# Optimization experiments

Measured on AMD Instinct MI355X. Metric: run time of the kernel, lower is better.

Reference implementation:

```python
import jax, jax.numpy as jnp
import numpy as np

N = 50000
E = 800000
IN_DIM = 256
HID = 64
HEADS = 4
OUT_DIM = 32
NEG_SLOPE = 0.2
EPS = 1e-5


def segment_softmax(logits, seg, num_segments):
    # logits: [E, H]; softmax over edges sharing the same destination node
    m = jax.ops.segment_max(logits, seg, num_segments=num_segments)
    m = jnp.where(jnp.isfinite(m), m, 0.0)
    e = jnp.exp(logits - m[seg])
    s = jax.ops.segment_sum(e, seg, num_segments=num_segments)
    return e / (s[seg] + 1e-16)


def setup_inputs() -> dict:
    key = jax.random.key(0)
    ks = jax.random.split(key, 16)
    d = {}
    d['x'] = jax.random.normal(ks[0], (N, IN_DIM), dtype=jnp.float32)
    d['edge_index'] = jax.random.randint(ks[1], (2, E), 0, N, dtype=jnp.int64)
    sc = lambda fan: 1.0 / np.sqrt(fan)
    # input transform: Linear(256->128), Linear(128->64)
    d['t1_w'] = jax.random.normal(ks[2], (IN_DIM, IN_DIM // 2), dtype=jnp.float32) * sc(IN_DIM)
    d['t1_b'] = jnp.zeros((IN_DIM // 2,), jnp.float32)
    d['t2_w'] = jax.random.normal(ks[3], (IN_DIM // 2, IN_DIM // 4), dtype=jnp.float32) * sc(IN_DIM // 2)
    d['t2_b'] = jnp.zeros((IN_DIM // 4,), jnp.float32)
    d['g1_w'] = jax.random.normal(ks[4], (IN_DIM // 4, HEADS * HID), dtype=jnp.float32) * sc(IN_DIM // 4)
    d['g1_att_src'] = jax.random.normal(ks[5], (HEADS, HID), dtype=jnp.float32) * sc(HID)
    d['g1_att_dst'] = jax.random.normal(ks[6], (HEADS, HID), dtype=jnp.float32) * sc(HID)
    d['g1_b'] = jnp.zeros((HEADS * HID,), jnp.float32)
    # GraphNorm(256)
    d['gn_w'] = jnp.ones((HEADS * HID,), jnp.float32)
    d['gn_b'] = jnp.zeros((HEADS * HID,), jnp.float32)
    d['gn_ms'] = jnp.ones((HEADS * HID,), jnp.float32)
    # GATConv 2: 256 -> 32, 1 head, no concat (mean == identity for 1 head)
    d['g2_w'] = jax.random.normal(ks[7], (HEADS * HID, OUT_DIM), dtype=jnp.float32) * sc(HEADS * HID)
    d['g2_att_src'] = jax.random.normal(ks[8], (1, OUT_DIM), dtype=jnp.float32) * sc(OUT_DIM)
    d['g2_att_dst'] = jax.random.normal(ks[9], (1, OUT_DIM), dtype=jnp.float32) * sc(OUT_DIM)
    d['g2_b'] = jnp.zeros((OUT_DIM,), jnp.float32)
    return d


def gat_conv(x, src, dst, w, att_src, att_dst, bias, n_nodes):
    heads, ch = att_src.shape
    h = (x @ w).reshape(n_nodes, heads, ch)            # [N,H,C]
    a_src = jnp.sum(h * att_src, axis=-1)              # [N,H]
    a_dst = jnp.sum(h * att_dst, axis=-1)              # [N,H]
    logits = jax.nn.leaky_relu(a_src[src] + a_dst[dst], NEG_SLOPE)  # [E,H]
    alpha = segment_softmax(logits, dst, n_nodes)      # [E,H]
    msgs = alpha[:, :, None] * h[src]                  # [E,H,C]
    out = jax.ops.segment_sum(msgs, dst, num_segments=n_nodes)  # [N,H,C]
    return out.reshape(n_nodes, heads * ch) + bias


def reference(x, edge_index, t1_w, t1_b, t2_w, t2_b,
              g1_w, g1_att_src, g1_att_dst, g1_b,
              gn_w, gn_b, gn_ms,
              g2_w, g2_att_src, g2_att_dst, g2_b):
    src, dst = edge_index[0], edge_index[1]
    # input transform (dropout inactive in eval)
    h = jax.nn.relu(x @ t1_w + t1_b)
    h = jax.nn.relu(h @ t2_w + t2_b)
    # GAT layer 1 (concat heads)
    h = gat_conv(h, src, dst, g1_w, g1_att_src, g1_att_dst, g1_b, N)
    # GraphNorm over the whole graph (batch=None -> single graph)
    mean = jnp.mean(h, axis=0)
    o = h - mean * gn_ms
    var = jnp.mean(o * o, axis=0)
    h = o / jnp.sqrt(var + EPS) * gn_w + gn_b
    h = jax.nn.elu(h)
    # GAT layer 2 (1 head, concat=False)
    h = gat_conv(h, src, dst, g2_w, g2_att_src, g2_att_dst, g2_b, N)
    return jax.nn.log_softmax(h, axis=1)
```

## Files before the change

### kernel.cpp

```cpp
#include <hip/hip_runtime.h>

#define NSLOPE 0.2f
#define GEPS 1e-5f

typedef unsigned short ushortT;
typedef __attribute__((ext_vector_type(8))) unsigned short us8;
typedef __attribute__((ext_vector_type(8))) __bf16 bf16x8;
typedef __attribute__((ext_vector_type(4))) float f32x4;

__device__ __forceinline__ float lrelu(float x) { return x >= 0.f ? x : NSLOPE * x; }
__device__ __forceinline__ ushortT f2bf(float f) {
    unsigned int u = __float_as_uint(f);
    return (ushortT)((u + 0x7fffu + ((u >> 16) & 1u)) >> 16);
}
__device__ __forceinline__ float bf2f(ushortT h) {
    return __uint_as_float((unsigned int)h << 16);
}
__device__ __forceinline__ ushortT f2h(float f) {
    union { _Float16 h; ushortT u; } v; v.h = (_Float16)f; return v.u;
}
__device__ __forceinline__ float h2f(ushortT u) {
    union { _Float16 h; ushortT u; } v; v.u = u; return (float)v.h;
}

__global__ __launch_bounds__(256) void k_prep_hist(
    const float* __restrict__ w1, const float* __restrict__ w2,
    const float* __restrict__ g1w, const float* __restrict__ g2w,
    ushortT* __restrict__ w1t, ushortT* __restrict__ w2t,
    ushortT* __restrict__ g1t, ushortT* __restrict__ g2t,
    const int* __restrict__ dst, int* __restrict__ deg, int E)
{
    if (blockIdx.x >= 128) {
        const int i = (blockIdx.x - 128) * 256 + threadIdx.x;
        if (i < E) atomicAdd(&deg[dst[i]], 1);
        return;
    }
    const int i = blockIdx.x * 256 + threadIdx.x;
    if (i < 128 * 256) { const int c = i >> 8, k = i & 255; w1t[i] = f2bf(w1[k * 128 + c]); }
    if (i < 64 * 128)  { const int c = i >> 7, k = i & 127; w2t[i] = f2bf(w2[k * 64 + c]); }
    if (i < 256 * 64)  { const int c = i >> 6, k = i & 63;  g1t[i] = f2bf(g1w[k * 256 + c]); }
    if (i < 32 * 256)  { const int c = i >> 8, k = i & 255; g2t[i] = f2bf(g2w[k * 32 + c]); }
}

__global__ __launch_bounds__(256) void k_lin1(const float* __restrict__ x,
    const ushortT* __restrict__ w1t, const float* __restrict__ b1,
    ushortT* __restrict__ h1, int n,
    const int* __restrict__ deg, int* __restrict__ offs, int* __restrict__ bsum, int gemmB)
{
    if ((int)blockIdx.x >= gemmB) {
        __shared__ int sm[256];
        const int t = threadIdx.x;
        const int i = (blockIdx.x - gemmB) * 256 + t;
        const int v = (i < n) ? deg[i] : 0;
        sm[t] = v;
        __syncthreads();
        for (int off = 1; off < 256; off <<= 1) {
            int add = (t >= off) ? sm[t - off] : 0;
            __syncthreads();
            sm[t] += add;
            __syncthreads();
        }
        if (i < n) offs[i] = sm[t] - v;
        if (t == 255) bsum[blockIdx.x - gemmB] = sm[255];
        return;
    }
    __shared__ us8 Ab[64 * 128 / 16];
    __shared__ us8 Bb[128 * 128 / 16];
    char* A = (char*)Ab; char* B = (char*)Bb;
    const int t = threadIdx.x;
    const int w = t >> 6, l = t & 63;
    const int lo = l & 15, hi = l >> 4;
    const int n0 = blockIdx.x * 64;
    const int wm = (w >> 1) * 32, wn = (w & 1) * 64;
    f32x4 acc[2][4];
    #pragma unroll
    for (int mf = 0; mf < 2; ++mf)
        #pragma unroll
        for (int nf = 0; nf < 4; ++nf) acc[mf][nf] = (f32x4){0.f, 0.f, 0.f, 0.f};

    const int arow = t >> 2, ak0 = (t & 3) * 16;
    int agn = n0 + arow; if (agn >= n) agn = n - 1;
    const int asw = (arow & 7) << 4;

    for (int kc = 0; kc < 4; ++kc) {
        __syncthreads();
        {
            ushortT tmp[16];
            const float* xp = &x[(size_t)agn * 256 + kc * 64 + ak0];
            #pragma unroll
            for (int j = 0; j < 4; ++j) {
                const float4 v = *(const float4*)(xp + j * 4);
                tmp[j*4+0] = f2bf(v.x); tmp[j*4+1] = f2bf(v.y);
                tmp[j*4+2] = f2bf(v.z); tmp[j*4+3] = f2bf(v.w);
            }
            *(us8*)(A + arow * 128 + ((ak0 * 2) ^ asw)) = *(us8*)tmp;
            *(us8*)(A + arow * 128 + ((ak0 * 2 + 16) ^ asw)) = *(us8*)(tmp + 8);
        }
        #pragma unroll
        for (int i = 0; i < 4; ++i) {
            const int idx = i * 256 + t, br = idx >> 3, bs = idx & 7;
            const us8 v = *(const us8*)&w1t[(size_t)br * 256 + kc * 64 + bs * 8];
            *(us8*)(B + br * 128 + ((bs * 16) ^ ((br & 7) << 4))) = v;
        }
        __syncthreads();
        #pragma unroll
        for (int ks = 0; ks < 2; ++ks) {
            const int koff = ks * 64 + hi * 16;
            bf16x8 af[2], bf[4];
            #pragma unroll
            for (int mf = 0; mf < 2; ++mf) {
                const int r = wm + mf * 16 + lo;
                af[mf] = *(const bf16x8*)(A + r * 128 + (koff ^ ((r & 7) << 4)));
            }
            #pragma unroll
            for (int nf = 0; nf < 4; ++nf) {
                const int r = wn + nf * 16 + lo;
                bf[nf] = *(const bf16x8*)(B + r * 128 + (koff ^ ((r & 7) << 4)));
            }
            #pragma unroll
            for (int mf = 0; mf < 2; ++mf)
                #pragma unroll
                for (int nf = 0; nf < 4; ++nf)
                    acc[mf][nf] = __builtin_amdgcn_mfma_f32_16x16x32_bf16(af[mf], bf[nf], acc[mf][nf], 0, 0, 0);
        }
    }
    #pragma unroll
    for (int nf = 0; nf < 4; ++nf) {
        const int col = wn + nf * 16 + lo;
        const float bb = b1[col];
        #pragma unroll
        for (int mf = 0; mf < 2; ++mf)
            #pragma unroll
            for (int j = 0; j < 4; ++j) {
                const int r = n0 + wm + mf * 16 + hi * 4 + j;
                if (r < n) h1[(size_t)r * 128 + col] = f2bf(fmaxf(acc[mf][nf][j] + bb, 0.f));
            }
    }
}

__global__ __launch_bounds__(256) void k_lin2(const ushortT* __restrict__ h1,
    const ushortT* __restrict__ w2t, const float* __restrict__ b2,
    ushortT* __restrict__ h2, int n,
    int* __restrict__ bsum, int nb, int gemmB)
{
    if ((int)blockIdx.x >= gemmB) {
        __shared__ int sm[256];
        const int t = threadIdx.x;
        const int v = (t < nb) ? bsum[t] : 0;
        sm[t] = v;
        __syncthreads();
        for (int off = 1; off < 256; off <<= 1) {
            int add = (t >= off) ? sm[t - off] : 0;
            __syncthreads();
            sm[t] += add;
            __syncthreads();
        }
        if (t < nb) bsum[t] = sm[t] - v;
        return;
    }
    __shared__ us8 Ab[64 * 128 / 16];
    __shared__ us8 Bb[64 * 128 / 16];
    char* A = (char*)Ab; char* B = (char*)Bb;
    const int t = threadIdx.x;
    const int w = t >> 6, l = t & 63;
    const int lo = l & 15, hi = l >> 4;
    const int n0 = blockIdx.x * 64;
    const int wm = (w >> 1) * 32, wn = (w & 1) * 32;
    f32x4 acc[2][2];
    #pragma unroll
    for (int mf = 0; mf < 2; ++mf)
        #pragma unroll
        for (int nf = 0; nf < 2; ++nf) acc[mf][nf] = (f32x4){0.f, 0.f, 0.f, 0.f};

    const int arow = t >> 2, ak0 = (t & 3) * 16;
    int agn = n0 + arow; if (agn >= n) agn = n - 1;
    const int asw = (arow & 7) << 4;

    for (int kc = 0; kc < 2; ++kc) {
        __syncthreads();
        {
            const us8 v0 = *(const us8*)&h1[(size_t)agn * 128 + kc * 64 + ak0];
            const us8 v1 = *(const us8*)&h1[(size_t)agn * 128 + kc * 64 + ak0 + 8];
            *(us8*)(A + arow * 128 + ((ak0 * 2) ^ asw)) = v0;
            *(us8*)(A + arow * 128 + ((ak0 * 2 + 16) ^ asw)) = v1;
        }
        #pragma unroll
        for (int i = 0; i < 2; ++i) {
            const int idx = i * 256 + t, br = idx >> 3, bs = idx & 7;
            const us8 v = *(const us8*)&w2t[(size_t)br * 128 + kc * 64 + bs * 8];
            *(us8*)(B + br * 128 + ((bs * 16) ^ ((br & 7) << 4))) = v;
        }
        __syncthreads();
        #pragma unroll
        for (int ks = 0; ks < 2; ++ks) {
            const int koff = ks * 64 + hi * 16;
            bf16x8 af[2], bf[2];
            #pragma unroll
            for (int mf = 0; mf < 2; ++mf) {
                const int r = wm + mf * 16 + lo;
                af[mf] = *(const bf16x8*)(A + r * 128 + (koff ^ ((r & 7) << 4)));
            }
            #pragma unroll
            for (int nf = 0; nf < 2; ++nf) {
                const int r = wn + nf * 16 + lo;
                bf[nf] = *(const bf16x8*)(B + r * 128 + (koff ^ ((r & 7) << 4)));
            }
            #pragma unroll
            for (int mf = 0; mf < 2; ++mf)
                #pragma unroll
                for (int nf = 0; nf < 2; ++nf)
                    acc[mf][nf] = __builtin_amdgcn_mfma_f32_16x16x32_bf16(af[mf], bf[nf], acc[mf][nf], 0, 0, 0);
        }
    }
    #pragma unroll
    for (int nf = 0; nf < 2; ++nf) {
        const int col = wn + nf * 16 + lo;
        const float bb = b2[col];
        #pragma unroll
        for (int mf = 0; mf < 2; ++mf)
            #pragma unroll
            for (int j = 0; j < 4; ++j) {
                const int r = n0 + wm + mf * 16 + hi * 4 + j;
                if (r < n) h2[(size_t)r * 64 + col] = f2bf(fmaxf(acc[mf][nf][j] + bb, 0.f));
            }
    }
}

__global__ __launch_bounds__(256) void k_g1feat(const ushortT* __restrict__ h2,
    const ushortT* __restrict__ g1t, const float* __restrict__ attS, const float* __restrict__ attD,
    ushortT* __restrict__ hg1, float* __restrict__ a1s, float* __restrict__ a1d, int n,
    int* __restrict__ offs, int* __restrict__ cursor, const int* __restrict__ bsum, int E, int gemmB)
{
    if ((int)blockIdx.x >= gemmB) {
        const int sb = blockIdx.x - gemmB;
        const int i = sb * 256 + threadIdx.x;
        if (i < n) {
            int o = offs[i] + bsum[i >> 8];
            offs[i] = o;
            cursor[i] = o;
        }
        if (i == 0) offs[n] = E;
        return;
    }
    __shared__ us8 Ab[64 * 128 / 16];
    __shared__ us8 Bb[256 * 128 / 16];
    char* A = (char*)Ab; char* B = (char*)Bb;
    const int t = threadIdx.x;
    const int w = t >> 6, l = t & 63;
    const int lo = l & 15, hi = l >> 4;
    const int n0 = blockIdx.x * 64;
    const int wm = (w >> 1) * 32, wn = (w & 1) * 128;
    f32x4 acc[2][8];
    #pragma unroll
    for (int mf = 0; mf < 2; ++mf)
        #pragma unroll
        for (int nf = 0; nf < 8; ++nf) acc[mf][nf] = (f32x4){0.f, 0.f, 0.f, 0.f};

    {
        const int arow = t >> 2, ak0 = (t & 3) * 16;
        int agn = n0 + arow; if (agn >= n) agn = n - 1;
        const int asw = (arow & 7) << 4;
        const us8 v0 = *(const us8*)&h2[(size_t)agn * 64 + ak0];
        const us8 v1 = *(const us8*)&h2[(size_t)agn * 64 + ak0 + 8];
        *(us8*)(A + arow * 128 + ((ak0 * 2) ^ asw)) = v0;
        *(us8*)(A + arow * 128 + ((ak0 * 2 + 16) ^ asw)) = v1;
    }
    #pragma unroll
    for (int i = 0; i < 8; ++i) {
        const int idx = i * 256 + t, br = idx >> 3, bs = idx & 7;
        const us8 v = *(const us8*)&g1t[(size_t)br * 64 + bs * 8];
        *(us8*)(B + br * 128 + ((bs * 16) ^ ((br & 7) << 4))) = v;
    }
    __syncthreads();
    #pragma unroll
    for (int ks = 0; ks < 2; ++ks) {
        const int koff = ks * 64 + hi * 16;
        bf16x8 af[2];
        #pragma unroll
        for (int mf = 0; mf < 2; ++mf) {
            const int r = wm + mf * 16 + lo;
            af[mf] = *(const bf16x8*)(A + r * 128 + (koff ^ ((r & 7) << 4)));
        }
        #pragma unroll
        for (int nf = 0; nf < 8; ++nf) {
            const int r = wn + nf * 16 + lo;
            const bf16x8 bf = *(const bf16x8*)(B + r * 128 + (koff ^ ((r & 7) << 4)));
            #pragma unroll
            for (int mf = 0; mf < 2; ++mf)
                acc[mf][nf] = __builtin_amdgcn_mfma_f32_16x16x32_bf16(af[mf], bf, acc[mf][nf], 0, 0, 0);
        }
    }
    float sS[8], sD[8];
    #pragma unroll
    for (int nf = 0; nf < 8; ++nf) {
        sS[nf] = attS[wn + nf * 16 + lo];
        sD[nf] = attD[wn + nf * 16 + lo];
    }
    const int hA = wn >> 6, hB = hA + 1;
    #pragma unroll
    for (int mf = 0; mf < 2; ++mf)
        #pragma unroll
        for (int j = 0; j < 4; ++j) {
            const int r = n0 + wm + mf * 16 + hi * 4 + j;
            float pSA = 0.f, pDA = 0.f, pSB = 0.f, pDB = 0.f;
            #pragma unroll
            for (int nf = 0; nf < 4; ++nf) {
                pSA = fmaf(acc[mf][nf][j], sS[nf], pSA);
                pDA = fmaf(acc[mf][nf][j], sD[nf], pDA);
                pSB = fmaf(acc[mf][nf + 4][j], sS[nf + 4], pSB);
                pDB = fmaf(acc[mf][nf + 4][j], sD[nf + 4], pDB);
            }
            #pragma unroll
            for (int off = 1; off < 16; off <<= 1) {
                pSA += __shfl_xor(pSA, off);
                pDA += __shfl_xor(pDA, off);
                pSB += __shfl_xor(pSB, off);
                pDB += __shfl_xor(pDB, off);
            }
            if (r < n) {
                if (lo == 0) {
                    a1s[r * 4 + hA] = pSA; a1s[r * 4 + hB] = pSB;
                    a1d[r * 4 + hA] = pDA; a1d[r * 4 + hB] = pDB;
                }
                #pragma unroll
                for (int nf = 0; nf < 8; ++nf)
                    hg1[(size_t)r * 256 + wn + nf * 16 + lo] = f2bf(acc[mf][nf][j]);
            }
        }
}

__global__ __launch_bounds__(256) void k_g2feat(const ushortT* __restrict__ out1,
    const float* __restrict__ cscale, const float* __restrict__ cshift,
    const ushortT* __restrict__ g2t, const float* __restrict__ attS, const float* __restrict__ attD,
    ushortT* __restrict__ hg2, float* __restrict__ a2s, float* __restrict__ a2d, int n)
{
    __shared__ us8 Ab[64 * 128 / 16];
    __shared__ us8 Bb[32 * 128 / 16];
    char* A = (char*)Ab; char* B = (char*)Bb;
    const int t = threadIdx.x;
    const int w = t >> 6, l = t & 63;
    const int lo = l & 15, hi = l >> 4;
    const int n0 = blockIdx.x * 64;
    const int wm = w * 16;
    f32x4 acc[2];
    acc[0] = (f32x4){0.f, 0.f, 0.f, 0.f};
    acc[1] = (f32x4){0.f, 0.f, 0.f, 0.f};

    const int arow = t >> 2, ak0 = (t & 3) * 16;
    int agn = n0 + arow; if (agn >= n) agn = n - 1;
    const int asw = (arow & 7) << 4;

    for (int kc = 0; kc < 4; ++kc) {
        __syncthreads();
        {
            ushortT tmp[16];
            const us8 v0 = *(const us8*)&out1[(size_t)agn * 256 + kc * 64 + ak0];
            const us8 v1 = *(const us8*)&out1[(size_t)agn * 256 + kc * 64 + ak0 + 8];
            #pragma unroll
            for (int j = 0; j < 8; ++j) {
                float a = bf2f(v0[j]) * cscale[kc * 64 + ak0 + j] + cshift[kc * 64 + ak0 + j];
                float b = bf2f(v1[j]) * cscale[kc * 64 + ak0 + 8 + j] + cshift[kc * 64 + ak0 + 8 + j];
                a = a > 0.f ? a : __expf(a) - 1.f;
                b = b > 0.f ? b : __expf(b) - 1.f;
                tmp[j] = f2bf(a); tmp[8 + j] = f2bf(b);
            }
            *(us8*)(A + arow * 128 + ((ak0 * 2) ^ asw)) = *(us8*)tmp;
            *(us8*)(A + arow * 128 + ((ak0 * 2 + 16) ^ asw)) = *(us8*)(tmp + 8);
        }
        {
            const int br = t >> 3, bs = t & 7;
            const us8 v = *(const us8*)&g2t[(size_t)br * 256 + kc * 64 + bs * 8];
            *(us8*)(B + br * 128 + ((bs * 16) ^ ((br & 7) << 4))) = v;
        }
        __syncthreads();
        #pragma unroll
        for (int ks = 0; ks < 2; ++ks) {
            const int koff = ks * 64 + hi * 16;
            const int ra = wm + lo;
            const bf16x8 af = *(const bf16x8*)(A + ra * 128 + (koff ^ ((ra & 7) << 4)));
            #pragma unroll
            for (int nf = 0; nf < 2; ++nf) {
                const int r = nf * 16 + lo;
                const bf16x8 bf = *(const bf16x8*)(B + r * 128 + (koff ^ ((r & 7) << 4)));
                acc[nf] = __builtin_amdgcn_mfma_f32_16x16x32_bf16(af, bf, acc[nf], 0, 0, 0);
            }
        }
    }
    float sS[2], sD[2];
    sS[0] = attS[lo]; sS[1] = attS[16 + lo];
    sD[0] = attD[lo]; sD[1] = attD[16 + lo];
    #pragma unroll
    for (int j = 0; j < 4; ++j) {
        const int r = n0 + wm + hi * 4 + j;
        float pS = fmaf(acc[0][j], sS[0], acc[1][j] * sS[1]);
        float pD = fmaf(acc[0][j], sD[0], acc[1][j] * sD[1]);
        #pragma unroll
        for (int off = 1; off < 16; off <<= 1) {
            pS += __shfl_xor(pS, off);
            pD += __shfl_xor(pD, off);
        }
        if (r < n) {
            if (lo == 0) { a2s[r] = pS; a2d[r] = pD; }
            hg2[(size_t)r * 32 + lo] = f2bf(acc[0][j]);
            hg2[(size_t)r * 32 + 16 + lo] = f2bf(acc[1][j]);
        }
    }
}

__global__ void k_scatter(const int* __restrict__ src, const int* __restrict__ dst,
                          int* __restrict__ cursor, int* __restrict__ csr, int e) {
    int i = blockIdx.x * 256 + threadIdx.x;
    if (i < e) {
        int p = atomicAdd(&cursor[dst[i]], 1);
        csr[p] = src[i];
    }
}

__global__ __launch_bounds__(256) void k_alpha1(
    const float* __restrict__ a1s, const float* __restrict__ a1d,
    const int* __restrict__ offs, const int* __restrict__ csr,
    ushortT* __restrict__ alphaH, int n)
{
    const int l = threadIdx.x & 15;
    const int d = blockIdx.x * 16 + (threadIdx.x >> 4);
    if (d >= n) return;
    const int start = offs[d], end = offs[d + 1];
    const float4* __restrict__ a1s4 = (const float4*)a1s;
    const float4 adv = ((const float4*)a1d)[d];
    const float ad0 = adv.x, ad1 = adv.y, ad2 = adv.z, ad3 = adv.w;

    float m0 = -1e30f, m1 = -1e30f, m2 = -1e30f, m3 = -1e30f;
    float s0 = 0.f, s1 = 0.f, s2 = 0.f, s3 = 0.f;
    for (int e = start + l; e < end; e += 16) {
        const float4 av = a1s4[csr[e]];
        const float l0 = lrelu(av.x + ad0), l1 = lrelu(av.y + ad1);
        const float l2 = lrelu(av.z + ad2), l3 = lrelu(av.w + ad3);
        float nm;
        nm = fmaxf(m0, l0); s0 = s0 * __expf(m0 - nm) + __expf(l0 - nm); m0 = nm;
        nm = fmaxf(m1, l1); s1 = s1 * __expf(m1 - nm) + __expf(l1 - nm); m1 = nm;
        nm = fmaxf(m2, l2); s2 = s2 * __expf(m2 - nm) + __expf(l2 - nm); m2 = nm;
        nm = fmaxf(m3, l3); s3 = s3 * __expf(m3 - nm) + __expf(l3 - nm); m3 = nm;
    }
    for (int off = 1; off < 16; off <<= 1) {
        float om, os, nm;
        om = __shfl_xor(m0, off, 16); os = __shfl_xor(s0, off, 16);
        nm = fmaxf(m0, om); s0 = s0 * __expf(m0 - nm) + os * __expf(om - nm); m0 = nm;
        om = __shfl_xor(m1, off, 16); os = __shfl_xor(s1, off, 16);
        nm = fmaxf(m1, om); s1 = s1 * __expf(m1 - nm) + os * __expf(om - nm); m1 = nm;
        om = __shfl_xor(m2, off, 16); os = __shfl_xor(s2, off, 16);
        nm = fmaxf(m2, om); s2 = s2 * __expf(m2 - nm) + os * __expf(om - nm); m2 = nm;
        om = __shfl_xor(m3, off, 16); os = __shfl_xor(s3, off, 16);
        nm = fmaxf(m3, om); s3 = s3 * __expf(m3 - nm) + os * __expf(om - nm); m3 = nm;
    }
    const float i0 = 1.f / (s0 + 1e-16f), i1 = 1.f / (s1 + 1e-16f);
    const float i2 = 1.f / (s2 + 1e-16f), i3 = 1.f / (s3 + 1e-16f);
    for (int e = start + l; e < end; e += 16) {
        const float4 av = a1s4[csr[e]];
        ushort4 o;
        o.x = f2h(__expf(lrelu(av.x + ad0) - m0) * i0);
        o.y = f2h(__expf(lrelu(av.y + ad1) - m1) * i1);
        o.z = f2h(__expf(lrelu(av.z + ad2) - m2) * i2);
        o.w = f2h(__expf(lrelu(av.w + ad3) - m3) * i3);
        *(ushort4*)&alphaH[(size_t)e * 4] = o;
    }
}

__global__ __launch_bounds__(256, 8) void k_pv1(
    const ushortT* __restrict__ hg1, const ushortT* __restrict__ alphaH,
    const int* __restrict__ offs, const int* __restrict__ csr,
    const float* __restrict__ bias, ushortT* __restrict__ out1, int n)
{
    const int lane = threadIdx.x & 63;
    const int d = blockIdx.x * 4 + (threadIdx.x >> 6);
    if (d >= n) return;
    const int start = offs[d], end = offs[d + 1];
    const int cg = lane & 31;
    const int c = cg * 8;
    const int es = lane >> 5;
    const int head = cg >> 3;
    float acc[8];
    #pragma unroll
    for (int j = 0; j < 8; ++j) acc[j] = 0.f;

    #pragma unroll 4
    for (int e = start + es; e < end; e += 2) {
        const int si = csr[e];
        const float al = h2f(alphaH[(size_t)e * 4 + head]);
        const us8 hv = *(const us8*)&hg1[(size_t)si * 256 + c];
        #pragma unroll
        for (int j = 0; j < 8; ++j) acc[j] = fmaf(al, bf2f(hv[j]), acc[j]);
    }
    #pragma unroll
    for (int j = 0; j < 8; ++j) acc[j] += __shfl_xor(acc[j], 32);
    if (es == 0) {
        const float4 b0 = *(const float4*)&bias[c];
        const float4 b1 = *(const float4*)&bias[c + 4];
        us8 o;
        o[0] = f2bf(acc[0] + b0.x); o[1] = f2bf(acc[1] + b0.y);
        o[2] = f2bf(acc[2] + b0.z); o[3] = f2bf(acc[3] + b0.w);
        o[4] = f2bf(acc[4] + b1.x); o[5] = f2bf(acc[5] + b1.y);
        o[6] = f2bf(acc[6] + b1.z); o[7] = f2bf(acc[7] + b1.w);
        *(us8*)&out1[(size_t)d * 256 + c] = o;
    }
}

__global__ __launch_bounds__(256) void k_colstat(const ushortT* __restrict__ out1,
    float* __restrict__ colsum, float* __restrict__ colsq, int n)
{
    const int t = threadIdx.x;
    float s = 0.f, q = 0.f;
    for (int r = blockIdx.x; r < n; r += gridDim.x) {
        const float v = bf2f(out1[(size_t)r * 256 + t]);
        s += v;
        q += v * v;
    }
    atomicAdd(&colsum[t], s);
    atomicAdd(&colsq[t], q);
}

__global__ void k_norm_params(const float* __restrict__ colsum, const float* __restrict__ colsq,
    const float* __restrict__ gw, const float* __restrict__ gb, const float* __restrict__ gms,
    float* __restrict__ scale, float* __restrict__ shift, int n)
{
    const int t = threadIdx.x;
    const float invn = 1.f / (float)n;
    const float mean = colsum[t] * invn;
    const float msq = colsq[t] * invn;
    const float ms = gms[t];
    const float var = msq - 2.f * ms * mean * mean + ms * ms * mean * mean;
    const float sc = gw[t] * rsqrtf(var + GEPS);
    scale[t] = sc;
    shift[t] = gb[t] - mean * ms * sc;
}

__global__ __launch_bounds__(256) void k_alpha2(
    const float* __restrict__ a2s, const float* __restrict__ a2d,
    const int* __restrict__ offs, const int* __restrict__ csr,
    ushortT* __restrict__ alphaH2, int n)
{
    const int l = threadIdx.x & 15;
    const int d = blockIdx.x * 16 + (threadIdx.x >> 4);
    if (d >= n) return;
    const int start = offs[d], end = offs[d + 1];
    const float adv = a2d[d];
    float m = -1e30f, s = 0.f;
    for (int e = start + l; e < end; e += 16) {
        const float lv = lrelu(a2s[csr[e]] + adv);
        const float nm = fmaxf(m, lv);
        s = s * __expf(m - nm) + __expf(lv - nm);
        m = nm;
    }
    for (int off = 1; off < 16; off <<= 1) {
        const float om = __shfl_xor(m, off, 16), os = __shfl_xor(s, off, 16);
        const float nm = fmaxf(m, om);
        s = s * __expf(m - nm) + os * __expf(om - nm);
        m = nm;
    }
    const float inv = 1.f / (s + 1e-16f);
    for (int e = start + l; e < end; e += 16)
        alphaH2[e] = f2h(__expf(lrelu(a2s[csr[e]] + adv) - m) * inv);
}

__global__ __launch_bounds__(256, 8) void k_pv2(
    const ushortT* __restrict__ hg2, const ushortT* __restrict__ alphaH2,
    const int* __restrict__ offs, const int* __restrict__ csr,
    const float* __restrict__ bias, float* __restrict__ out, int n)
{
    const int lane = threadIdx.x & 31;
    const int d = blockIdx.x * 8 + (threadIdx.x >> 5);
    if (d >= n) return;
    const int start = offs[d], end = offs[d + 1];
    const int l = lane & 15, es = lane >> 4;
    const int c = l * 2;
    float acc0 = 0.f, acc1 = 0.f;
    #pragma unroll 4
    for (int e = start + es; e < end; e += 2) {
        const int si = csr[e];
        const float al = h2f(alphaH2[e]);
        const ushort2 hv = *(const ushort2*)&hg2[(size_t)si * 32 + c];
        acc0 = fmaf(al, bf2f(hv.x), acc0);
        acc1 = fmaf(al, bf2f(hv.y), acc1);
    }
    acc0 += __shfl_xor(acc0, 16, 32);
    acc1 += __shfl_xor(acc1, 16, 32);
    const float v0 = acc0 + bias[c];
    const float v1 = acc1 + bias[c + 1];
    float mx = fmaxf(v0, v1);
    for (int off = 1; off < 16; off <<= 1) mx = fmaxf(mx, __shfl_xor(mx, off, 16));
    float se = __expf(v0 - mx) + __expf(v1 - mx);
    for (int off = 1; off < 16; off <<= 1) se += __shfl_xor(se, off, 16);
    const float ls = __logf(se);
    if (es == 0) {
        float2 o = {v0 - mx - ls, v1 - mx - ls};
        *(float2*)&out[(size_t)d * 32 + c] = o;
    }
}

extern "C" void kernel_launch(void* const* d_in, const int* in_sizes, int n_in,
                              void* d_out, int out_size, void* d_ws, size_t ws_size,
                              hipStream_t stream)
{
    const float* x    = (const float*)d_in[0];
    const int*   ei   = (const int*)d_in[1];
    const float* t1w  = (const float*)d_in[2];
    const float* t1b  = (const float*)d_in[3];
    const float* t2w  = (const float*)d_in[4];
    const float* t2b  = (const float*)d_in[5];
    const float* g1w  = (const float*)d_in[6];
    const float* g1as = (const float*)d_in[7];
    const float* g1ad = (const float*)d_in[8];
    const float* g1b  = (const float*)d_in[9];
    const float* gnw  = (const float*)d_in[10];
    const float* gnb  = (const float*)d_in[11];
    const float* gnms = (const float*)d_in[12];
    const float* g2w  = (const float*)d_in[13];
    const float* g2as = (const float*)d_in[14];
    const float* g2ad = (const float*)d_in[15];
    const float* g2b  = (const float*)d_in[16];

    const int N = in_sizes[0] / 256;
    const int E = in_sizes[1] / 2;
    const int* srcA = ei;
    const int* dstA = ei + E;

    char* ws = (char*)d_ws;
    size_t cur = 0;
    auto alloc = [&](size_t bytes) -> char* {
        char* p = ws + cur;
        cur += (bytes + 255) & ~(size_t)255;
        return p;
    };
    ushortT* h1      = (ushortT*)alloc((size_t)N * 128 * 2);
    ushortT* h2      = (ushortT*)alloc((size_t)N * 64 * 2);
    ushortT* hg1     = (ushortT*)alloc((size_t)N * 256 * 2);
    float*   a1s     = (float*)alloc((size_t)N * 4 * 4);
    float*   a1d     = (float*)alloc((size_t)N * 4 * 4);
    ushortT* out1    = (ushortT*)alloc((size_t)N * 256 * 2);
    ushortT* hg2     = (ushortT*)alloc((size_t)N * 32 * 2);
    float*   a2s     = (float*)alloc((size_t)N * 4);
    float*   a2d     = (float*)alloc((size_t)N * 4);
    int*     deg     = (int*)alloc((size_t)(N + 1) * 4);
    int*     offs    = (int*)alloc((size_t)(N + 1) * 4);
    int*     cursor  = (int*)alloc((size_t)N * 4);
    int*     bsum    = (int*)alloc(1024);
    int*     csr     = (int*)alloc((size_t)E * 4);
    ushortT* alphaH  = (ushortT*)alloc((size_t)E * 4 * 2);
    ushortT* alphaH2 = (ushortT*)alloc((size_t)E * 2);
    float*   colsum  = (float*)alloc(1024);
    float*   colsq   = (float*)alloc(1024);
    float*   cscale  = (float*)alloc(1024);
    float*   cshift  = (float*)alloc(1024);
    ushortT* w1t     = (ushortT*)alloc(128 * 256 * 2);
    ushortT* w2t     = (ushortT*)alloc(64 * 128 * 2);
    ushortT* g1t     = (ushortT*)alloc(256 * 64 * 2);
    ushortT* g2t     = (ushortT*)alloc(32 * 256 * 2);

    hipMemsetAsync(deg, 0, (size_t)(N + 1) * 4, stream);
    hipMemsetAsync(colsum, 0, 2048, stream);

    const int EB  = (E + 255) / 256;
    const int NB  = (N + 255) / 256;
    const int B64 = (N + 63) / 64;
    const int B16 = (N + 15) / 16;
    const int B8  = (N + 7) / 8;
    const int B4  = (N + 3) / 4;

    k_prep_hist<<<128 + EB, 256, 0, stream>>>(t1w, t2w, g1w, g2w, w1t, w2t, g1t, g2t, dstA, deg, E);
    k_lin1<<<B64 + NB, 256, 0, stream>>>(x, w1t, t1b, h1, N, deg, offs, bsum, B64);
    k_lin2<<<B64 + 1, 256, 0, stream>>>(h1, w2t, t2b, h2, N, bsum, NB, B64);
    k_g1feat<<<B64 + NB, 256, 0, stream>>>(h2, g1t, g1as, g1ad, hg1, a1s, a1d, N, offs, cursor, bsum, E, B64);
    k_scatter<<<EB, 256, 0, stream>>>(srcA, dstA, cursor, csr, E);
    k_alpha1<<<B16, 256, 0, stream>>>(a1s, a1d, offs, csr, alphaH, N);
    k_pv1<<<B4, 256, 0, stream>>>(hg1, alphaH, offs, csr, g1b, out1, N);
    k_colstat<<<256, 256, 0, stream>>>(out1, colsum, colsq, N);
    k_norm_params<<<1, 256, 0, stream>>>(colsum, colsq, gnw, gnb, gnms, cscale, cshift, N);
    k_g2feat<<<B64, 256, 0, stream>>>(out1, cscale, cshift, g2t, g2as, g2ad, hg2, a2s, a2d, N);
    k_alpha2<<<B16, 256, 0, stream>>>(a2s, a2d, offs, csr, alphaH2, N);
    k_pv2<<<B8, 256, 0, stream>>>(hg2, alphaH2, offs, csr, g2b, (float*)d_out, N);
}
```

Measured before the change: 305.7 us.

## Fuse column stats into pv1, norm params into g2feat, alpha2 into pv2

Column sum and sum-of-squares for GraphNorm now accumulate inside the layer-1 aggregation kernel through per-block shared-memory partials and atomics, removing the separate k_colstat pass over out1. The scale/shift computation moves into the prologue of k_g2feat, which drops the single-block k_norm_params launch. Layer-2 softmax is computed inside k_pv2, which recomputes alpha per edge on the fly instead of writing and rereading an alpha array. Layer-1 alpha is stored as fp32 rather than fp16, doubling that buffer's traffic in exchange for dropping the conversions. The stats are taken from fp32 values before bf16 rounding, so they differ slightly from the previous version.

```diff
diff --git a/kernel.cpp b/kernel.cpp
--- a/kernel.cpp
+++ b/kernel.cpp
@@ -15,12 +15,6 @@
 }
 __device__ __forceinline__ float bf2f(ushortT h) {
     return __uint_as_float((unsigned int)h << 16);
-}
-__device__ __forceinline__ ushortT f2h(float f) {
-    union { _Float16 h; ushortT u; } v; v.h = (_Float16)f; return v.u;
-}
-__device__ __forceinline__ float h2f(ushortT u) {
-    union { _Float16 h; ushortT u; } v; v.u = u; return (float)v.h;
 }
 
 __global__ __launch_bounds__(256) void k_prep_hist(
@@ -330,18 +324,30 @@
 }
 
 __global__ __launch_bounds__(256) void k_g2feat(const ushortT* __restrict__ out1,
-    const float* __restrict__ cscale, const float* __restrict__ cshift,
+    const float* __restrict__ colsum, const float* __restrict__ colsq,
+    const float* __restrict__ gw, const float* __restrict__ gb, const float* __restrict__ gms,
     const ushortT* __restrict__ g2t, const float* __restrict__ attS, const float* __restrict__ attD,
     ushortT* __restrict__ hg2, float* __restrict__ a2s, float* __restrict__ a2d, int n)
 {
     __shared__ us8 Ab[64 * 128 / 16];
     __shared__ us8 Bb[32 * 128 / 16];
+    __shared__ float lsc[256], lsh[256];
     char* A = (char*)Ab; char* B = (char*)Bb;
     const int t = threadIdx.x;
     const int w = t >> 6, l = t & 63;
     const int lo = l & 15, hi = l >> 4;
     const int n0 = blockIdx.x * 64;
     const int wm = w * 16;
+    {
+        const float invn = 1.f / (float)n;
+        const float mean = colsum[t] * invn;
+        const float msq = colsq[t] * invn;
+        const float ms = gms[t];
+        const float var = msq - 2.f * ms * mean * mean + ms * ms * mean * mean;
+        const float sc = gw[t] * rsqrtf(var + GEPS);
+        lsc[t] = sc;
+        lsh[t] = gb[t] - mean * ms * sc;
+    }
     f32x4 acc[2];
     acc[0] = (f32x4){0.f, 0.f, 0.f, 0.f};
     acc[1] = (f32x4){0.f, 0.f, 0.f, 0.f};
@@ -358,8 +364,8 @@
             const us8 v1 = *(const us8*)&out1[(size_t)agn * 256 + kc * 64 + ak0 + 8];
             #pragma unroll
             for (int j = 0; j < 8; ++j) {
-                float a = bf2f(v0[j]) * cscale[kc * 64 + ak0 + j] + cshift[kc * 64 + ak0 + j];
-                float b = bf2f(v1[j]) * cscale[kc * 64 + ak0 + 8 + j] + cshift[kc * 64 + ak0 + 8 + j];
+                float a = bf2f(v0[j]) * lsc[kc * 64 + ak0 + j] + lsh[kc * 64 + ak0 + j];
+                float b = bf2f(v1[j]) * lsc[kc * 64 + ak0 + 8 + j] + lsh[kc * 64 + ak0 + 8 + j];
                 a = a > 0.f ? a : __expf(a) - 1.f;
                 b = b > 0.f ? b : __expf(b) - 1.f;
                 tmp[j] = f2bf(a); tmp[8 + j] = f2bf(b);
@@ -419,7 +425,7 @@
 __global__ __launch_bounds__(256) void k_alpha1(
     const float* __restrict__ a1s, const float* __restrict__ a1d,
     const int* __restrict__ offs, const int* __restrict__ csr,
-    ushortT* __restrict__ alphaH, int n)
+    float* __restrict__ alphaE, int n)
 {
     const int l = threadIdx.x & 15;
     const int d = blockIdx.x * 16 + (threadIdx.x >> 4);
@@ -456,127 +462,104 @@
     const float i2 = 1.f / (s2 + 1e-16f), i3 = 1.f / (s3 + 1e-16f);
     for (int e = start + l; e < end; e += 16) {
         const float4 av = a1s4[csr[e]];
-        ushort4 o;
-        o.x = f2h(__expf(lrelu(av.x + ad0) - m0) * i0);
-        o.y = f2h(__expf(lrelu(av.y + ad1) - m1) * i1);
-        o.z = f2h(__expf(lrelu(av.z + ad2) - m2) * i2);
-        o.w = f2h(__expf(lrelu(av.w + ad3) - m3) * i3);
-        *(ushort4*)&alphaH[(size_t)e * 4] = o;
+        float4 o;
+        o.x = __expf(lrelu(av.x + ad0) - m0) * i0;
+        o.y = __expf(lrelu(av.y + ad1) - m1) * i1;
+        o.z = __expf(lrelu(av.z + ad2) - m2) * i2;
+        o.w = __expf(lrelu(av.w + ad3) - m3) * i3;
+        *(float4*)&alphaE[(size_t)e * 4] = o;
     }
 }
 
 __global__ __launch_bounds__(256, 8) void k_pv1(
-    const ushortT* __restrict__ hg1, const ushortT* __restrict__ alphaH,
+    const ushortT* __restrict__ hg1, const float* __restrict__ alphaE,
     const int* __restrict__ offs, const int* __restrict__ csr,
-    const float* __restrict__ bias, ushortT* __restrict__ out1, int n)
-{
-    const int lane = threadIdx.x & 63;
-    const int d = blockIdx.x * 4 + (threadIdx.x >> 6);
-    if (d >= n) return;
-    const int start = offs[d], end = offs[d + 1];
+    const float* __restrict__ bias, ushortT* __restrict__ out1,
+    float* __restrict__ colsum, float* __restrict__ colsq, int n)
+{
+    __shared__ float scs[4][256], scq[4][256];
+    const int tid = threadIdx.x;
+    const int lane = tid & 63, w = tid >> 6;
+    const int d = blockIdx.x * 4 + w;
     const int cg = lane & 31;
     const int c = cg * 8;
     const int es = lane >> 5;
     const int head = cg >> 3;
-    float acc[8];
-    #pragma unroll
-    for (int j = 0; j < 8; ++j) acc[j] = 0.f;
-
-    #pragma unroll 4
-    for (int e = start + es; e < end; e += 2) {
-        const int si = csr[e];
-        const float al = h2f(alphaH[(size_t)e * 4 + head]);
-        const us8 hv = *(const us8*)&hg1[(size_t)si * 256 + c];
-        #pragma unroll
-        for (int j = 0; j < 8; ++j) acc[j] = fmaf(al, bf2f(hv[j]), acc[j]);
-    }
-    #pragma unroll
-    for (int j = 0; j < 8; ++j) acc[j] += __shfl_xor(acc[j], 32);
-    if (es == 0) {
-        const float4 b0 = *(const float4*)&bias[c];
-        const float4 b1 = *(const float4*)&bias[c + 4];
-        us8 o;
-        o[0] = f2bf(acc[0] + b0.x); o[1] = f2bf(acc[1] + b0.y);
-        o[2] = f2bf(acc[2] + b0.z); o[3] = f2bf(acc[3] + b0.w);
-        o[4] = f2bf(acc[4] + b1.x); o[5] = f2bf(acc[5] + b1.y);
-        o[6] = f2bf(acc[6] + b1.z); o[7] = f2bf(acc[7] + b1.w);
-        *(us8*)&out1[(size_t)d * 256 + c] = o;
-    }
-}
-
-__global__ __launch_bounds__(256) void k_colstat(const ushortT* __restrict__ out1,
-    float* __restrict__ colsum, float* __restrict__ colsq, int n)
-{
-    const int t = threadIdx.x;
-    float s = 0.f, q = 0.f;
-    for (int r = blockIdx.x; r < n; r += gridDim.x) {
-        const float v = bf2f(out1[(size_t)r * 256 + t]);
-        s += v;
-        q += v * v;
-    }
-    atomicAdd(&colsum[t], s);
-    atomicAdd(&colsq[t], q);
-}
-
-__global__ void k_norm_params(const float* __restrict__ colsum, const float* __restrict__ colsq,
-    const float* __restrict__ gw, const float* __restrict__ gb, const float* __restrict__ gms,
-    float* __restrict__ scale, float* __restrict__ shift, int n)
-{
-    const int t = threadIdx.x;
-    const float invn = 1.f / (float)n;
-    const float mean = colsum[t] * invn;
-    const float msq = colsq[t] * invn;
-    const float ms = gms[t];
-    const float var = msq - 2.f * ms * mean * mean + ms * ms * mean * mean;
-    const float sc = gw[t] * rsqrtf(var + GEPS);
-    scale[t] = sc;
-    shift[t] = gb[t] - mean * ms * sc;
-}
-
-__global__ __launch_bounds__(256) void k_alpha2(
-    const float* __restrict__ a2s, const float* __restrict__ a2d,
+    #pragma unroll
+    for (int q = 0; q < 4; ++q) { scs[q][tid] = 0.f; scq[q][tid] = 0.f; }
+    __syncthreads();
+
+    if (d < n) {
+        const int start = offs[d], end = offs[d + 1];
+        float acc[8];
+        #pragma unroll
+        for (int j = 0; j < 8; ++j) acc[j] = 0.f;
+
+        #pragma unroll 4
+        for (int e = start + es; e < end; e += 2) {
+            const int si = csr[e];
+            const float al = alphaE[(size_t)e * 4 + head];
+            const us8 hv = *(const us8*)&hg1[(size_t)si * 256 + c];
+            #pragma unroll
+            for (int j = 0; j < 8; ++j) acc[j] = fmaf(al, bf2f(hv[j]), acc[j]);
+        }
+        #pragma unroll
+        for (int j = 0; j < 8; ++j) acc[j] += __shfl_xor(acc[j], 32);
+        if (es == 0) {
+            const float4 b0 = *(const float4*)&bias[c];
+            const float4 b1 = *(const float4*)&bias[c + 4];
+            float v[8];
+            v[0] = acc[0] + b0.x; v[1] = acc[1] + b0.y; v[2] = acc[2] + b0.z; v[3] = acc[3] + b0.w;
+            v[4] = acc[4] + b1.x; v[5] = acc[5] + b1.y; v[6] = acc[6] + b1.z; v[7] = acc[7] + b1.w;
+            us8 o;
+            #pragma unroll
+            for (int j = 0; j < 8; ++j) o[j] = f2bf(v[j]);
+            *(us8*)&out1[(size_t)d * 256 + c] = o;
+            #pragma unroll
+            for (int j = 0; j < 8; ++j) {
+                scs[w][c + j] = v[j];
+                scq[w][c + j] = v[j] * v[j];
+            }
+        }
+    }
+    __syncthreads();
+    const float s4 = scs[0][tid] + scs[1][tid] + scs[2][tid] + scs[3][tid];
+    const float q4 = scq[0][tid] + scq[1][tid] + scq[2][tid] + scq[3][tid];
+    atomicAdd(&colsum[tid], s4);
+    atomicAdd(&colsq[tid], q4);
+}
+
+__global__ __launch_bounds__(256, 8) void k_pv2(
+    const ushortT* __restrict__ hg2, const float* __restrict__ a2s, const float* __restrict__ a2d,
     const int* __restrict__ offs, const int* __restrict__ csr,
-    ushortT* __restrict__ alphaH2, int n)
-{
-    const int l = threadIdx.x & 15;
-    const int d = blockIdx.x * 16 + (threadIdx.x >> 4);
+    const float* __restrict__ bias, float* __restrict__ out, int n)
+{
+    const int lane = threadIdx.x & 31;
+    const int d = blockIdx.x * 8 + (threadIdx.x >> 5);
     if (d >= n) return;
     const int start = offs[d], end = offs[d + 1];
     const float adv = a2d[d];
     float m = -1e30f, s = 0.f;
-    for (int e = start + l; e < end; e += 16) {
+    for (int e = start + lane; e < end; e += 32) {
         const float lv = lrelu(a2s[csr[e]] + adv);
         const float nm = fmaxf(m, lv);
         s = s * __expf(m - nm) + __expf(lv - nm);
         m = nm;
     }
-    for (int off = 1; off < 16; off <<= 1) {
-        const float om = __shfl_xor(m, off, 16), os = __shfl_xor(s, off, 16);
+    for (int off = 1; off < 32; off <<= 1) {
+        const float om = __shfl_xor(m, off, 32), os = __shfl_xor(s, off, 32);
         const float nm = fmaxf(m, om);
         s = s * __expf(m - nm) + os * __expf(om - nm);
         m = nm;
     }
     const float inv = 1.f / (s + 1e-16f);
-    for (int e = start + l; e < end; e += 16)
-        alphaH2[e] = f2h(__expf(lrelu(a2s[csr[e]] + adv) - m) * inv);
-}
-
-__global__ __launch_bounds__(256, 8) void k_pv2(
-    const ushortT* __restrict__ hg2, const ushortT* __restrict__ alphaH2,
-    const int* __restrict__ offs, const int* __restrict__ csr,
-    const float* __restrict__ bias, float* __restrict__ out, int n)
-{
-    const int lane = threadIdx.x & 31;
-    const int d = blockIdx.x * 8 + (threadIdx.x >> 5);
-    if (d >= n) return;
-    const int start = offs[d], end = offs[d + 1];
     const int l = lane & 15, es = lane >> 4;
     const int c = l * 2;
     float acc0 = 0.f, acc1 = 0.f;
     #pragma unroll 4
     for (int e = start + es; e < end; e += 2) {
         const int si = csr[e];
-        const float al = h2f(alphaH2[e]);
+        const float al = __expf(lrelu(a2s[si] + adv) - m) * inv;
         const ushort2 hv = *(const ushort2*)&hg2[(size_t)si * 32 + c];
         acc0 = fmaf(al, bf2f(hv.x), acc0);
         acc1 = fmaf(al, bf2f(hv.y), acc1);
@@ -644,12 +627,9 @@
     int*     cursor  = (int*)alloc((size_t)N * 4);
     int*     bsum    = (int*)alloc(1024);
     int*     csr     = (int*)alloc((size_t)E * 4);
-    ushortT* alphaH  = (ushortT*)alloc((size_t)E * 4 * 2);
-    ushortT* alphaH2 = (ushortT*)alloc((size_t)E * 2);
+    float*   alphaE  = (float*)alloc((size_t)E * 4 * 4);
     float*   colsum  = (float*)alloc(1024);
     float*   colsq   = (float*)alloc(1024);
-    float*   cscale  = (float*)alloc(1024);
-    float*   cshift  = (float*)alloc(1024);
     ushortT* w1t     = (ushortT*)alloc(128 * 256 * 2);
     ushortT* w2t     = (ushortT*)alloc(64 * 128 * 2);
     ushortT* g1t     = (ushortT*)alloc(256 * 64 * 2);
@@ -670,11 +650,8 @@
     k_lin2<<<B64 + 1, 256, 0, stream>>>(h1, w2t, t2b, h2, N, bsum, NB, B64);
     k_g1feat<<<B64 + NB, 256, 0, stream>>>(h2, g1t, g1as, g1ad, hg1, a1s, a1d, N, offs, cursor, bsum, E, B64);
     k_scatter<<<EB, 256, 0, stream>>>(srcA, dstA, cursor, csr, E);
-    k_alpha1<<<B16, 256, 0, stream>>>(a1s, a1d, offs, csr, alphaH, N);
-    k_pv1<<<B4, 256, 0, stream>>>(hg1, alphaH, offs, csr, g1b, out1, N);
-    k_colstat<<<256, 256, 0, stream>>>(out1, colsum, colsq, N);
-    k_norm_params<<<1, 256, 0, stream>>>(colsum, colsq, gnw, gnb, gnms, cscale, cshift, N);
-    k_g2feat<<<B64, 256, 0, stream>>>(out1, cscale, cshift, g2t, g2as, g2ad, hg2, a2s, a2d, N);
-    k_alpha2<<<B16, 256, 0, stream>>>(a2s, a2d, offs, csr, alphaH2, N);
-    k_pv2<<<B8, 256, 0, stream>>>(hg2, alphaH2, offs, csr, g2b, (float*)d_out, N);
-}
+    k_alpha1<<<B16, 256, 0, stream>>>(a1s, a1d, offs, csr, alphaE, N);
+    k_pv1<<<B4, 256, 0, stream>>>(hg1, alphaE, offs, csr, g1b, out1, colsum, colsq, N);
+    k_g2feat<<<B64, 256, 0, stream>>>(out1, colsum, colsq, gnw, gnb, gnms, g2t, g2as, g2ad, hg2, a2s, a2d, N);
+    k_pv2<<<B8, 256, 0, stream>>>(hg2, a2s, a2d, offs, csr, g2b, (float*)d_out, N);
+}
```

Result: slower. 503.0 us (+64.5%).
